# Kernel tuning notes

Hardware: AMD Instinct MI355X
Metric: run time of the kernel (lower is better)

The kernel has to match this reference:

```python
import jax, jax.numpy as jnp
import numpy as np

B, S, D, H, DH, TLEN, TD = 4, 1024, 1024, 16, 64, 256, 256
EPS = 1e-5


def layer_norm(x, g, b):
    m = jnp.mean(x, axis=-1, keepdims=True)
    v = jnp.mean((x - m) ** 2, axis=-1, keepdims=True)
    return (x - m) * jax.lax.rsqrt(v + EPS) * g + b


def rotate_half(x):
    x1, x2 = jnp.split(x, 2, axis=-1)
    return jnp.concatenate((-x2, x1), axis=-1)


def apply_rope(pos, t):
    # pos: [S, DH] -> [1, S, 1, DH]; t: [B, S, H, DH]
    p = pos[None, :, None, :]
    return t * jnp.cos(p) + rotate_half(t) * jnp.sin(p)


def mha(q_in, kv_in, in_w, in_b, out_w, out_b, n_heads):
    # standard nn.MultiheadAttention math (batch-first tensors here)
    d = q_in.shape[-1]
    dh = d // n_heads
    q = q_in @ in_w[:d].T + in_b[:d]
    k = kv_in @ in_w[d:2 * d].T + in_b[d:2 * d]
    v = kv_in @ in_w[2 * d:].T + in_b[2 * d:]
    q = q.reshape(q.shape[0], q.shape[1], n_heads, dh)
    k = k.reshape(k.shape[0], k.shape[1], n_heads, dh)
    v = v.reshape(v.shape[0], v.shape[1], n_heads, dh)
    scores = jnp.einsum('bihd,bjhd->bhij', q, k) / jnp.sqrt(jnp.asarray(dh, q.dtype))
    attn = jax.nn.softmax(scores, axis=-1)
    o = jnp.einsum('bhij,bjhd->bihd', attn, v)
    o = o.reshape(o.shape[0], o.shape[1], d)
    return o @ out_w.T + out_b


def setup_inputs():
    key = jax.random.key(0)
    ks = jax.random.split(key, 20)
    s = 0.02
    inp = {
        'x': jax.random.normal(ks[0], (B, S, D), jnp.float32),
        'text_emb': jax.random.normal(ks[1], (B, TLEN, D), jnp.float32),
        'time_emb': jax.random.normal(ks[2], (B, TD), jnp.float32),
    }
    # true RoPE position encoding, matching RotaryEmbedding.forward
    inv_freq = 1.0 / (10000 ** (jnp.arange(0, DH, 2, dtype=jnp.float32) / DH))
    freqs = jnp.arange(S, dtype=jnp.float32)[:, None] * inv_freq[None, :]
    inp['rotary_pos'] = jnp.concatenate((freqs, freqs), axis=-1)  # [S, DH]
    inp.update(
        ln1_g=jnp.ones((D,), jnp.float32), ln1_b=jnp.zeros((D,), jnp.float32),
        ln2_g=jnp.ones((D,), jnp.float32), ln2_b=jnp.zeros((D,), jnp.float32),
        ln3_g=jnp.ones((D,), jnp.float32), ln3_b=jnp.zeros((D,), jnp.float32),
        attn_in_w=jax.random.normal(ks[3], (3 * D, D), jnp.float32) * s,
        attn_in_b=jnp.zeros((3 * D,), jnp.float32),
        ca_in_w=jax.random.normal(ks[4], (3 * D, D), jnp.float32) * s,
        ca_in_b=jnp.zeros((3 * D,), jnp.float32),
        ca_out_w=jax.random.normal(ks[5], (D, D), jnp.float32) * s,
        ca_out_b=jnp.zeros((D,), jnp.float32),
        fc1_w=jax.random.normal(ks[6], (4 * D, D), jnp.float32) * s,
        fc1_b=jnp.zeros((4 * D,), jnp.float32),
        gate_w=jax.random.normal(ks[7], (4 * D, D), jnp.float32) * s,
        gate_b=jnp.zeros((4 * D,), jnp.float32),
        fc2_w=jax.random.normal(ks[8], (D, 4 * D), jnp.float32) * s,
        fc2_b=jnp.zeros((D,), jnp.float32),
    )
    return inp


def reference(x, text_emb, time_emb, rotary_pos,
              ln1_g, ln1_b, ln2_g, ln2_b, ln3_g, ln3_b,
              attn_in_w, attn_in_b,
              ca_in_w, ca_in_b, ca_out_w, ca_out_b,
              fc1_w, fc1_b, gate_w, gate_b, fc2_w, fc2_b):
    b, n, d = x.shape
    # --- self-attention with manual RoPE (NOTE: original skips out_proj) ---
    residual = x
    xn = layer_norm(x, ln1_g, ln1_b)
    q = xn @ attn_in_w[:d].T + attn_in_b[:d]
    k = xn @ attn_in_w[d:2 * d].T + attn_in_b[d:2 * d]
    v = xn @ attn_in_w[2 * d:].T + attn_in_b[2 * d:]
    q = q.reshape(b, n, H, DH)
    k = k.reshape(b, n, H, DH)
    v = v.reshape(b, n, H, DH)
    q = apply_rope(rotary_pos, q)
    k = apply_rope(rotary_pos, k)
    scores = jnp.einsum('bihd,bjhd->bhij', q, k) / jnp.sqrt(jnp.asarray(DH, x.dtype))
    attn = jax.nn.softmax(scores, axis=-1)
    attn_out = jnp.einsum('bhij,bjhd->bihd', attn, v).reshape(b, n, d)
    x = attn_out + residual
    # --- cross-attention (full MHA, dropout inactive at eval) ---
    residual = x
    xn = layer_norm(x, ln2_g, ln2_b)
    x = mha(xn, text_emb, ca_in_w, ca_in_b, ca_out_w, ca_out_b, H) + residual
    # --- gated MLP ---
    residual = x
    xn = layer_norm(x, ln3_g, ln3_b)
    h = jax.nn.gelu(xn @ fc1_w.T + fc1_b, approximate=False)
    g = jax.nn.sigmoid(xn @ gate_w.T + gate_b)
    return (h * g) @ fc2_w.T + fc2_b + residual
```

## Files before the change

### kernel.cpp

```cpp
#include <hip/hip_runtime.h>
#include <hip/hip_bf16.h>

#define SEQ 1024
#define DIM 1024
#define NH 16

typedef __bf16 bf16_t;
typedef __bf16 bf16x8 __attribute__((ext_vector_type(8)));
typedef __bf16 bf16x4 __attribute__((ext_vector_type(4)));
typedef float f32x4 __attribute__((ext_vector_type(4)));

__device__ __forceinline__ f32x4 mfma16(bf16x8 a, bf16x8 b, f32x4 c) {
    return __builtin_amdgcn_mfma_f32_16x16x32_bf16(a, b, c, 0, 0, 0);
}

__device__ __forceinline__ void gload16(const bf16_t* g, bf16_t* l) {
    __builtin_amdgcn_global_load_lds(
        (const __attribute__((address_space(1))) void*)g,
        (__attribute__((address_space(3))) void*)l, 16, 0, 0);
}

enum { EPI_BF16 = 0, EPI_F32_RESID = 1, EPI_BF16_GELU = 2, EPI_BF16_SIGMUL = 3 };

__global__ __launch_bounds__(256) void cvt_kernel(const float* __restrict__ in,
                                                  bf16_t* __restrict__ out) {
    const int i = blockIdx.x * 256 + threadIdx.x;
    const float4 v = ((const float4*)in)[i];
    bf16x4 o = {(bf16_t)v.x, (bf16_t)v.y, (bf16_t)v.z, (bf16_t)v.w};
    ((bf16x4*)out)[i] = o;
}

__global__ __launch_bounds__(256) void ln_kernel(const float* __restrict__ in,
                                                 const float* __restrict__ g,
                                                 const float* __restrict__ bsh,
                                                 bf16_t* __restrict__ out) {
    __shared__ float red[4], red2[4];
    const int row = blockIdx.x, tid = threadIdx.x;
    const float4 v = ((const float4*)(in + (size_t)row * DIM))[tid];
    float s = v.x + v.y + v.z + v.w;
#pragma unroll
    for (int o = 32; o; o >>= 1) s += __shfl_down(s, o, 64);
    if ((tid & 63) == 0) red[tid >> 6] = s;
    __syncthreads();
    const float mean = (red[0] + red[1] + red[2] + red[3]) * (1.0f / DIM);
    const float dx = v.x - mean, dy = v.y - mean, dz = v.z - mean, dw = v.w - mean;
    float s2 = dx * dx + dy * dy + dz * dz + dw * dw;
#pragma unroll
    for (int o = 32; o; o >>= 1) s2 += __shfl_xor(s2, o, 64);
    if ((tid & 63) == 0) red2[tid >> 6] = s2;
    __syncthreads();
    const float var = (red2[0] + red2[1] + red2[2] + red2[3]) * (1.0f / DIM);
    const float rs = rsqrtf(var + 1e-5f);
    const float4 gv = ((const float4*)g)[tid];
    const float4 bv = ((const float4*)bsh)[tid];
    bf16x4 o4 = {(bf16_t)(dx * rs * gv.x + bv.x), (bf16_t)(dy * rs * gv.y + bv.y),
                 (bf16_t)(dz * rs * gv.z + bv.z), (bf16_t)(dw * rs * gv.w + bv.w)};
    ((bf16x4*)(out + (size_t)row * DIM))[tid] = o4;
}

__global__ __launch_bounds__(256) void rope_kernel(bf16_t* __restrict__ qkv,
                                                   const float* __restrict__ rp) {
    const int t = blockIdx.x * 256 + threadIdx.x;
    const int row = t >> 9;
    const int rem = t & 511;
    const int h = rem >> 5, d = rem & 31;
    const int s = row & (SEQ - 1);
    const float p0 = rp[s * 64 + d];
    const float p1 = rp[s * 64 + d + 32];
    float s0, c0, s1, c1;
    sincosf(p0, &s0, &c0);
    sincosf(p1, &s1, &c1);
    const size_t base = (size_t)row * 3072 + h * 64 + d;
#pragma unroll
    for (int off = 0; off <= 1024; off += 1024) {
        const float a = (float)qkv[base + off];
        const float b = (float)qkv[base + off + 32];
        qkv[base + off] = (bf16_t)(a * c0 - b * s0);
        qkv[base + off + 32] = (bf16_t)(b * c1 + a * s1);
    }
}

__device__ __forceinline__ float epi_apply_gelu(float v) {
    return 0.5f * v * (1.0f + erff(v * 0.70710678118f));
}

template <int EPI>
__global__ __launch_bounds__(512, 4) void gemm8w(
    const bf16_t* __restrict__ A, int lda, const bf16_t* __restrict__ W, int ldw,
    const float* __restrict__ bias, const void* __restrict__ aux,
    void* __restrict__ outv, int ldo, int K, int nM) {
    __shared__ bf16_t As[2][8192];
    __shared__ bf16_t Bs[2][8192];
    const int tid = threadIdx.x;
    const int wave = tid >> 6, lane = tid & 63;
    const int wm = wave >> 2, wn = wave & 3;
    const int lr = lane & 15, hi = lane >> 4;

    const int q = gridDim.x >> 3;
    const int t = (blockIdx.x & 7) * q + (blockIdx.x >> 3);
    const int rowA0 = (t % nM) * 128;
    const int rowB0 = (t / nM) * 128;

    f32x4 acc[4][2];
#pragma unroll
    for (int m = 0; m < 4; ++m)
#pragma unroll
        for (int n = 0; n < 2; ++n) acc[m][n] = (f32x4){0.f, 0.f, 0.f, 0.f};

    const int c0 = wave * 2;
    auto stage = [&](int kt, int b) {
        const int k0 = kt * 64;
#pragma unroll
        for (int u = 0; u < 2; ++u) {
            const int c = c0 + u, s = c >> 1, ks = c & 1;
            const int grow = s * 16 + lr, gcol = k0 + ks * 32 + hi * 8;
            gload16(A + (size_t)(rowA0 + grow) * lda + gcol, &As[b][c * 512]);
            gload16(W + (size_t)(rowB0 + grow) * ldw + gcol, &Bs[b][c * 512]);
        }
    };

    const int NT = K >> 6;
    stage(0, 0);
    __syncthreads();

    for (int kt = 0; kt < NT; ++kt) {
        const int cur = kt & 1;
        if (kt + 1 < NT) stage(kt + 1, cur ^ 1);
#pragma unroll
        for (int ks = 0; ks < 2; ++ks) {
            bf16x8 af[4], bfr[2];
#pragma unroll
            for (int mf = 0; mf < 4; ++mf)
                af[mf] = *(const bf16x8*)&As[cur][((wm * 4 + mf) * 2 + ks) * 512 +
                                                 hi * 128 + lr * 8];
#pragma unroll
            for (int nf = 0; nf < 2; ++nf)
                bfr[nf] = *(const bf16x8*)&Bs[cur][((wn * 2 + nf) * 2 + ks) * 512 +
                                                  hi * 128 + lr * 8];
#pragma unroll
            for (int mf = 0; mf < 4; ++mf)
#pragma unroll
                for (int nf = 0; nf < 2; ++nf)
                    acc[mf][nf] = mfma16(af[mf], bfr[nf], acc[mf][nf]);
        }
        __syncthreads();
    }

    float bn[2];
#pragma unroll
    for (int n = 0; n < 2; ++n) bn[n] = bias[rowB0 + wn * 32 + n * 16 + lr];
#pragma unroll
    for (int m = 0; m < 4; ++m) {
#pragma unroll
        for (int j = 0; j < 4; ++j) {
            const int row = rowA0 + wm * 64 + m * 16 + hi * 4 + j;
#pragma unroll
            for (int n = 0; n < 2; ++n) {
                const int col = rowB0 + wn * 32 + n * 16 + lr;
                float val = acc[m][n][j] + bn[n];
                const size_t oidx = (size_t)row * ldo + col;
                if constexpr (EPI == EPI_BF16) {
                    ((bf16_t*)outv)[oidx] = (bf16_t)val;
                } else if constexpr (EPI == EPI_F32_RESID) {
                    ((float*)outv)[oidx] = val + ((const float*)aux)[oidx];
                } else if constexpr (EPI == EPI_BF16_GELU) {
                    ((bf16_t*)outv)[oidx] = (bf16_t)epi_apply_gelu(val);
                } else {
                    const float sg = 1.0f / (1.0f + expf(-val));
                    ((bf16_t*)outv)[oidx] =
                        (bf16_t)(sg * (float)((const bf16_t*)aux)[oidx]);
                }
            }
        }
    }
}

#define ALD 72
template <bool OUTBF>
__global__ __launch_bounds__(256) void attn_kernel(
    const bf16_t* __restrict__ qp, int ldq, int qoff,
    const bf16_t* __restrict__ kp, int ldk, int koff,
    const bf16_t* __restrict__ vp, int ldv, int voff, int skv,
    const float* __restrict__ resid, void* __restrict__ outp, float scale) {
    __shared__ bf16_t Ks[64 * ALD];
    __shared__ bf16_t Vt[64 * ALD];
    __shared__ bf16_t Ps[4 * 16 * ALD];
    const int b = blockIdx.z, h = blockIdx.y, qt = blockIdx.x;
    const int tid = threadIdx.x;
    const int wave = tid >> 6, lane = tid & 63;
    const int lr = lane & 15, hi = lane >> 4;

    const size_t qrow = (size_t)(b * SEQ + qt * 64 + wave * 16 + lr);
    const bf16_t* qb = qp + qrow * ldq + qoff + h * 64;
    const bf16x8 qf0 = *(const bf16x8*)(qb + hi * 8);
    const bf16x8 qf1 = *(const bf16x8*)(qb + 32 + hi * 8);

    f32x4 oacc[4];
#pragma unroll
    for (int n = 0; n < 4; ++n) oacc[n] = (f32x4){0.f, 0.f, 0.f, 0.f};
    float mrun[4] = {-1e30f, -1e30f, -1e30f, -1e30f};
    float lrun[4] = {0.f, 0.f, 0.f, 0.f};

    bf16_t* pw = &Ps[wave * 16 * ALD];
    const int nkt = skv >> 6;
    for (int kt = 0; kt < nkt; ++kt) {
#pragma unroll
        for (int t = 0; t < 2; ++t) {
            const int idx = t * 256 + tid;
            const int key = idx >> 3, c8 = (idx & 7) * 8;
            const size_t krow = (size_t)(b * skv + kt * 64 + key);
            bf16x8 kv = *(const bf16x8*)(kp + krow * ldk + koff + h * 64 + c8);
            *(bf16x8*)&Ks[key * ALD + c8] = kv;
            bf16x8 vv = *(const bf16x8*)(vp + krow * ldv + voff + h * 64 + c8);
#pragma unroll
            for (int i = 0; i < 8; ++i) Vt[(c8 + i) * ALD + key] = vv[i];
        }
        __syncthreads();

        f32x4 s[4];
#pragma unroll
        for (int n = 0; n < 4; ++n) {
            f32x4 z = (f32x4){0.f, 0.f, 0.f, 0.f};
            z = mfma16(qf0, *(const bf16x8*)&Ks[(n * 16 + lr) * ALD + hi * 8], z);
            z = mfma16(qf1, *(const bf16x8*)&Ks[(n * 16 + lr) * ALD + 32 + hi * 8], z);
            s[n] = z * scale;
        }
        float alpha[4];
#pragma unroll
        for (int j = 0; j < 4; ++j) {
            float mt = fmaxf(fmaxf(s[0][j], s[1][j]), fmaxf(s[2][j], s[3][j]));
#pragma unroll
            for (int o = 8; o >= 1; o >>= 1) mt = fmaxf(mt, __shfl_xor(mt, o, 64));
            const float mnew = fmaxf(mrun[j], mt);
            alpha[j] = expf(mrun[j] - mnew);
            float rsum = 0.f;
#pragma unroll
            for (int n = 0; n < 4; ++n) {
                const float p = expf(s[n][j] - mnew);
                s[n][j] = p;
                rsum += p;
            }
#pragma unroll
            for (int o = 8; o >= 1; o >>= 1) rsum += __shfl_xor(rsum, o, 64);
            lrun[j] = lrun[j] * alpha[j] + rsum;
            mrun[j] = mnew;
        }
#pragma unroll
        for (int j = 0; j < 4; ++j) {
            const int pr = hi * 4 + j;
#pragma unroll
            for (int n = 0; n < 4; ++n) pw[pr * ALD + n * 16 + lr] = (bf16_t)s[n][j];
        }
#pragma unroll
        for (int n = 0; n < 4; ++n)
#pragma unroll
            for (int j = 0; j < 4; ++j) oacc[n][j] *= alpha[j];
#pragma unroll
        for (int ks = 0; ks < 2; ++ks) {
            const bf16x8 pa = *(const bf16x8*)&pw[lr * ALD + ks * 32 + hi * 8];
#pragma unroll
            for (int n = 0; n < 4; ++n) {
                const bf16x8 vf = *(const bf16x8*)&Vt[(n * 16 + lr) * ALD + ks * 32 + hi * 8];
                oacc[n] = mfma16(pa, vf, oacc[n]);
            }
        }
        __syncthreads();
    }

    const size_t orow0 = (size_t)(b * SEQ + qt * 64 + wave * 16);
#pragma unroll
    for (int n = 0; n < 4; ++n) {
#pragma unroll
        for (int j = 0; j < 4; ++j) {
            const int r = hi * 4 + j;
            const size_t idx = (orow0 + r) * DIM + h * 64 + n * 16 + lr;
            float val = oacc[n][j] / lrun[j];
            if constexpr (OUTBF) {
                ((bf16_t*)outp)[idx] = (bf16_t)val;
            } else {
                ((float*)outp)[idx] = val + resid[idx];
            }
        }
    }
}

extern "C" void kernel_launch(void* const* d_in, const int* in_sizes, int n_in,
                              void* d_out, int out_size, void* d_ws, size_t ws_size,
                              hipStream_t stream) {
    const float* x = (const float*)d_in[0];
    const float* text_emb = (const float*)d_in[1];
    const float* rotary = (const float*)d_in[3];
    const float* ln1_g = (const float*)d_in[4];
    const float* ln1_b = (const float*)d_in[5];
    const float* ln2_g = (const float*)d_in[6];
    const float* ln2_b = (const float*)d_in[7];
    const float* ln3_g = (const float*)d_in[8];
    const float* ln3_b = (const float*)d_in[9];
    const float* attn_in_w = (const float*)d_in[10];
    const float* attn_in_b = (const float*)d_in[11];
    const float* ca_in_w = (const float*)d_in[12];
    const float* ca_in_b = (const float*)d_in[13];
    const float* ca_out_w = (const float*)d_in[14];
    const float* ca_out_b = (const float*)d_in[15];
    const float* fc1_w = (const float*)d_in[16];
    const float* fc1_b = (const float*)d_in[17];
    const float* gate_w = (const float*)d_in[18];
    const float* gate_b = (const float*)d_in[19];
    const float* fc2_w = (const float*)d_in[20];
    const float* fc2_b = (const float*)d_in[21];

    char* ws = (char*)d_ws;
    bf16_t* attn_w_bf = (bf16_t*)(ws);
    bf16_t* ca_in_bf = (bf16_t*)(ws + 6291456);
    bf16_t* ca_out_bf = (bf16_t*)(ws + 12582912);
    bf16_t* fc1_bf = (bf16_t*)(ws + 14680064);
    bf16_t* gate_bf = (bf16_t*)(ws + 23068672);
    bf16_t* fc2_bf = (bf16_t*)(ws + 31457280);
    bf16_t* text_bf = (bf16_t*)(ws + 39845888);
    bf16_t* xn = (bf16_t*)(ws + 41943040);
    float* xA = (float*)(ws + 50331648);
    char* S = ws + 67108864;
    bf16_t* qkv = (bf16_t*)S;
    bf16_t* cq = (bf16_t*)S;
    bf16_t* ckv = (bf16_t*)(S + 8388608);
    bf16_t* ca_attn = (bf16_t*)(S + 12582912);
    bf16_t* hbuf = (bf16_t*)S;
    float* out = (float*)d_out;

    cvt_kernel<<<3072, 256, 0, stream>>>(attn_in_w, attn_w_bf);
    cvt_kernel<<<3072, 256, 0, stream>>>(ca_in_w, ca_in_bf);
    cvt_kernel<<<1024, 256, 0, stream>>>(ca_out_w, ca_out_bf);
    cvt_kernel<<<4096, 256, 0, stream>>>(fc1_w, fc1_bf);
    cvt_kernel<<<4096, 256, 0, stream>>>(gate_w, gate_bf);
    cvt_kernel<<<4096, 256, 0, stream>>>(fc2_w, fc2_bf);
    cvt_kernel<<<1024, 256, 0, stream>>>(text_emb, text_bf);

    ln_kernel<<<4096, 256, 0, stream>>>(x, ln1_g, ln1_b, xn);
    gemm8w<EPI_BF16><<<768, 512, 0, stream>>>(
        xn, 1024, attn_w_bf, 1024, attn_in_b, nullptr, qkv, 3072, 1024, 32);
    rope_kernel<<<8192, 256, 0, stream>>>(qkv, rotary);
    attn_kernel<false><<<dim3(16, 16, 4), 256, 0, stream>>>(
        qkv, 3072, 0, qkv, 3072, 1024, qkv, 3072, 2048, 1024, x, xA, 0.125f);

    ln_kernel<<<4096, 256, 0, stream>>>(xA, ln2_g, ln2_b, xn);
    gemm8w<EPI_BF16><<<256, 512, 0, stream>>>(
        xn, 1024, ca_in_bf, 1024, ca_in_b, nullptr, cq, 1024, 1024, 32);
    gemm8w<EPI_BF16><<<128, 512, 0, stream>>>(
        text_bf, 1024, ca_in_bf + (size_t)1024 * 1024, 1024, ca_in_b + 1024, nullptr,
        ckv, 2048, 1024, 8);
    attn_kernel<true><<<dim3(16, 16, 4), 256, 0, stream>>>(
        cq, 1024, 0, ckv, 2048, 0, ckv, 2048, 1024, 256, nullptr, ca_attn, 0.125f);
    gemm8w<EPI_F32_RESID><<<256, 512, 0, stream>>>(
        ca_attn, 1024, ca_out_bf, 1024, ca_out_b, xA, xA, 1024, 1024, 32);

    ln_kernel<<<4096, 256, 0, stream>>>(xA, ln3_g, ln3_b, xn);
    gemm8w<EPI_BF16_GELU><<<1024, 512, 0, stream>>>(
        xn, 1024, fc1_bf, 1024, fc1_b, nullptr, hbuf, 4096, 1024, 32);
    gemm8w<EPI_BF16_SIGMUL><<<1024, 512, 0, stream>>>(
        xn, 1024, gate_bf, 1024, gate_b, hbuf, hbuf, 4096, 1024, 32);
    gemm8w<EPI_F32_RESID><<<256, 512, 0, stream>>>(
        hbuf, 4096, fc2_bf, 4096, fc2_b, xA, out, 1024, 4096, 32);
}
```

Measured before the change: 569.8 us.

## Pre-transpose V and stream K/V tiles into LDS via direct global loads

Adds a separate kernel that transposes V per head into a [b,h,d,s] buffer, so the attention kernel no longer performs scalar transposed LDS stores per tile. The new attention kernel loads K and V tiles with global_load_lds in an MFMA-friendly swizzled layout, remaps block indices for better L2 locality across heads, and switches to fast __expf. This adds an extra kernel launch and a round trip through global memory for V, and the direct LDS loads are not double-buffered.

```diff
diff --git a/kernel.cpp b/kernel.cpp
--- a/kernel.cpp
+++ b/kernel.cpp
@@ -82,6 +82,148 @@
 
 __device__ __forceinline__ float epi_apply_gelu(float v) {
     return 0.5f * v * (1.0f + erff(v * 0.70710678118f));
+}
+
+__global__ __launch_bounds__(256) void vtrans_kernel(
+    const bf16_t* __restrict__ src, int ld, int voff, int skv,
+    bf16_t* __restrict__ vt) {
+    __shared__ bf16_t T[64 * 72];
+    const int qt = blockIdx.x, h = blockIdx.y, b = blockIdx.z;
+    const int tid = threadIdx.x;
+    const int s0 = qt * 64;
+#pragma unroll
+    for (int t = 0; t < 2; ++t) {
+        const int idx = t * 256 + tid;
+        const int r = idx >> 3, c8 = (idx & 7) * 8;
+        bf16x8 v = *(const bf16x8*)(src + (size_t)(b * skv + s0 + r) * ld +
+                                    voff + h * 64 + c8);
+        *(bf16x8*)&T[r * 72 + c8] = v;
+    }
+    __syncthreads();
+    const size_t base = ((size_t)(b * NH + h) * 64) * skv;
+#pragma unroll
+    for (int t = 0; t < 2; ++t) {
+        const int idx = t * 256 + tid;
+        const int d = idx >> 3, s8 = (idx & 7) * 8;
+        bf16x8 w;
+#pragma unroll
+        for (int i = 0; i < 8; ++i) w[i] = T[(s8 + i) * 72 + d];
+        *(bf16x8*)(vt + base + (size_t)d * skv + s0 + s8) = w;
+    }
+}
+
+#define ALD 72
+template <bool OUTBF>
+__global__ __launch_bounds__(256) void attn2_kernel(
+    const bf16_t* __restrict__ qp, int ldq, int qoff,
+    const bf16_t* __restrict__ kp, int ldk, int koff,
+    const bf16_t* __restrict__ vtp, int skv,
+    const float* __restrict__ resid, void* __restrict__ outp, float scale) {
+    __shared__ bf16_t Ks[4096];
+    __shared__ bf16_t Vs[4096];
+    __shared__ bf16_t Ps[4 * 16 * ALD];
+    const int nwg = gridDim.x;
+    const int t = (blockIdx.x & 7) * (nwg >> 3) + (blockIdx.x >> 3);
+    const int qt = t & 15;
+    const int bh = t >> 4;
+    const int b = bh >> 4, h = bh & 15;
+    const int tid = threadIdx.x;
+    const int wave = tid >> 6, lane = tid & 63;
+    const int lr = lane & 15, hi = lane >> 4;
+
+    const size_t qrow = (size_t)(b * SEQ + qt * 64 + wave * 16 + lr);
+    const bf16_t* qb = qp + qrow * ldq + qoff + h * 64;
+    const bf16x8 qf0 = *(const bf16x8*)(qb + hi * 8);
+    const bf16x8 qf1 = *(const bf16x8*)(qb + 32 + hi * 8);
+
+    const bf16_t* vbase = vtp + ((size_t)bh * 64) * skv;
+
+    f32x4 oacc[4];
+#pragma unroll
+    for (int n = 0; n < 4; ++n) oacc[n] = (f32x4){0.f, 0.f, 0.f, 0.f};
+    float mrun[4] = {-1e30f, -1e30f, -1e30f, -1e30f};
+    float lrun[4] = {0.f, 0.f, 0.f, 0.f};
+
+    bf16_t* pw = &Ps[wave * 16 * ALD];
+    const int nkt = skv >> 6;
+    for (int kt = 0; kt < nkt; ++kt) {
+#pragma unroll
+        for (int u = 0; u < 2; ++u) {
+            const int c = wave * 2 + u;
+            const int grow = wave * 16 + lr, gcol = u * 32 + hi * 8;
+            gload16(kp + (size_t)(b * skv + kt * 64 + grow) * ldk + koff +
+                        h * 64 + gcol,
+                    &Ks[c * 512]);
+            gload16(vbase + (size_t)grow * skv + kt * 64 + gcol, &Vs[c * 512]);
+        }
+        __syncthreads();
+
+        f32x4 s[4];
+#pragma unroll
+        for (int n = 0; n < 4; ++n) {
+            f32x4 z = (f32x4){0.f, 0.f, 0.f, 0.f};
+            z = mfma16(qf0, *(const bf16x8*)&Ks[(n * 2 + 0) * 512 + hi * 128 + lr * 8], z);
+            z = mfma16(qf1, *(const bf16x8*)&Ks[(n * 2 + 1) * 512 + hi * 128 + lr * 8], z);
+            s[n] = z * scale;
+        }
+        float alpha[4];
+#pragma unroll
+        for (int j = 0; j < 4; ++j) {
+            float mt = fmaxf(fmaxf(s[0][j], s[1][j]), fmaxf(s[2][j], s[3][j]));
+#pragma unroll
+            for (int o = 8; o >= 1; o >>= 1) mt = fmaxf(mt, __shfl_xor(mt, o, 64));
+            const float mnew = fmaxf(mrun[j], mt);
+            alpha[j] = __expf(mrun[j] - mnew);
+            float rsum = 0.f;
+#pragma unroll
+            for (int n = 0; n < 4; ++n) {
+                const float p = __expf(s[n][j] - mnew);
+                s[n][j] = p;
+                rsum += p;
+            }
+#pragma unroll
+            for (int o = 8; o >= 1; o >>= 1) rsum += __shfl_xor(rsum, o, 64);
+            lrun[j] = lrun[j] * alpha[j] + rsum;
+            mrun[j] = mnew;
+        }
+#pragma unroll
+        for (int j = 0; j < 4; ++j) {
+            const int pr = hi * 4 + j;
+#pragma unroll
+            for (int n = 0; n < 4; ++n) pw[pr * ALD + n * 16 + lr] = (bf16_t)s[n][j];
+        }
+#pragma unroll
+        for (int n = 0; n < 4; ++n)
+#pragma unroll
+            for (int j = 0; j < 4; ++j) oacc[n][j] *= alpha[j];
+#pragma unroll
+        for (int ks = 0; ks < 2; ++ks) {
+            const bf16x8 pa = *(const bf16x8*)&pw[lr * ALD + ks * 32 + hi * 8];
+#pragma unroll
+            for (int n = 0; n < 4; ++n) {
+                const bf16x8 vf =
+                    *(const bf16x8*)&Vs[(n * 2 + ks) * 512 + hi * 128 + lr * 8];
+                oacc[n] = mfma16(pa, vf, oacc[n]);
+            }
+        }
+        __syncthreads();
+    }
+
+    const size_t orow0 = (size_t)(b * SEQ + qt * 64 + wave * 16);
+#pragma unroll
+    for (int n = 0; n < 4; ++n) {
+#pragma unroll
+        for (int j = 0; j < 4; ++j) {
+            const int r = hi * 4 + j;
+            const size_t idx = (orow0 + r) * DIM + h * 64 + n * 16 + lr;
+            float val = oacc[n][j] / lrun[j];
+            if constexpr (OUTBF) {
+                ((bf16_t*)outp)[idx] = (bf16_t)val;
+            } else {
+                ((float*)outp)[idx] = val + resid[idx];
+            }
+        }
+    }
 }
 
 template <int EPI>
@@ -170,115 +312,6 @@
                     ((bf16_t*)outv)[oidx] =
                         (bf16_t)(sg * (float)((const bf16_t*)aux)[oidx]);
                 }
-            }
-        }
-    }
-}
-
-#define ALD 72
-template <bool OUTBF>
-__global__ __launch_bounds__(256) void attn_kernel(
-    const bf16_t* __restrict__ qp, int ldq, int qoff,
-    const bf16_t* __restrict__ kp, int ldk, int koff,
-    const bf16_t* __restrict__ vp, int ldv, int voff, int skv,
-    const float* __restrict__ resid, void* __restrict__ outp, float scale) {
-    __shared__ bf16_t Ks[64 * ALD];
-    __shared__ bf16_t Vt[64 * ALD];
-    __shared__ bf16_t Ps[4 * 16 * ALD];
-    const int b = blockIdx.z, h = blockIdx.y, qt = blockIdx.x;
-    const int tid = threadIdx.x;
-    const int wave = tid >> 6, lane = tid & 63;
-    const int lr = lane & 15, hi = lane >> 4;
-
-    const size_t qrow = (size_t)(b * SEQ + qt * 64 + wave * 16 + lr);
-    const bf16_t* qb = qp + qrow * ldq + qoff + h * 64;
-    const bf16x8 qf0 = *(const bf16x8*)(qb + hi * 8);
-    const bf16x8 qf1 = *(const bf16x8*)(qb + 32 + hi * 8);
-
-    f32x4 oacc[4];
-#pragma unroll
-    for (int n = 0; n < 4; ++n) oacc[n] = (f32x4){0.f, 0.f, 0.f, 0.f};
-    float mrun[4] = {-1e30f, -1e30f, -1e30f, -1e30f};
-    float lrun[4] = {0.f, 0.f, 0.f, 0.f};
-
-    bf16_t* pw = &Ps[wave * 16 * ALD];
-    const int nkt = skv >> 6;
-    for (int kt = 0; kt < nkt; ++kt) {
-#pragma unroll
-        for (int t = 0; t < 2; ++t) {
-            const int idx = t * 256 + tid;
-            const int key = idx >> 3, c8 = (idx & 7) * 8;
-            const size_t krow = (size_t)(b * skv + kt * 64 + key);
-            bf16x8 kv = *(const bf16x8*)(kp + krow * ldk + koff + h * 64 + c8);
-            *(bf16x8*)&Ks[key * ALD + c8] = kv;
-            bf16x8 vv = *(const bf16x8*)(vp + krow * ldv + voff + h * 64 + c8);
-#pragma unroll
-            for (int i = 0; i < 8; ++i) Vt[(c8 + i) * ALD + key] = vv[i];
-        }
-        __syncthreads();
-
-        f32x4 s[4];
-#pragma unroll
-        for (int n = 0; n < 4; ++n) {
-            f32x4 z = (f32x4){0.f, 0.f, 0.f, 0.f};
-            z = mfma16(qf0, *(const bf16x8*)&Ks[(n * 16 + lr) * ALD + hi * 8], z);
-            z = mfma16(qf1, *(const bf16x8*)&Ks[(n * 16 + lr) * ALD + 32 + hi * 8], z);
-            s[n] = z * scale;
-        }
-        float alpha[4];
-#pragma unroll
-        for (int j = 0; j < 4; ++j) {
-            float mt = fmaxf(fmaxf(s[0][j], s[1][j]), fmaxf(s[2][j], s[3][j]));
-#pragma unroll
-            for (int o = 8; o >= 1; o >>= 1) mt = fmaxf(mt, __shfl_xor(mt, o, 64));
-            const float mnew = fmaxf(mrun[j], mt);
-            alpha[j] = expf(mrun[j] - mnew);
-            float rsum = 0.f;
-#pragma unroll
-            for (int n = 0; n < 4; ++n) {
-                const float p = expf(s[n][j] - mnew);
-                s[n][j] = p;
-                rsum += p;
-            }
-#pragma unroll
-            for (int o = 8; o >= 1; o >>= 1) rsum += __shfl_xor(rsum, o, 64);
-            lrun[j] = lrun[j] * alpha[j] + rsum;
-            mrun[j] = mnew;
-        }
-#pragma unroll
-        for (int j = 0; j < 4; ++j) {
-            const int pr = hi * 4 + j;
-#pragma unroll
-            for (int n = 0; n < 4; ++n) pw[pr * ALD + n * 16 + lr] = (bf16_t)s[n][j];
-        }
-#pragma unroll
-        for (int n = 0; n < 4; ++n)
-#pragma unroll
-            for (int j = 0; j < 4; ++j) oacc[n][j] *= alpha[j];
-#pragma unroll
-        for (int ks = 0; ks < 2; ++ks) {
-            const bf16x8 pa = *(const bf16x8*)&pw[lr * ALD + ks * 32 + hi * 8];
-#pragma unroll
-            for (int n = 0; n < 4; ++n) {
-                const bf16x8 vf = *(const bf16x8*)&Vt[(n * 16 + lr) * ALD + ks * 32 + hi * 8];
-                oacc[n] = mfma16(pa, vf, oacc[n]);
-            }
-        }
-        __syncthreads();
-    }
-
-    const size_t orow0 = (size_t)(b * SEQ + qt * 64 + wave * 16);
-#pragma unroll
-    for (int n = 0; n < 4; ++n) {
-#pragma unroll
-        for (int j = 0; j < 4; ++j) {
-            const int r = hi * 4 + j;
-            const size_t idx = (orow0 + r) * DIM + h * 64 + n * 16 + lr;
-            float val = oacc[n][j] / lrun[j];
-            if constexpr (OUTBF) {
-                ((bf16_t*)outp)[idx] = (bf16_t)val;
-            } else {
-                ((float*)outp)[idx] = val + resid[idx];
             }
         }
     }
@@ -321,9 +354,11 @@
     float* xA = (float*)(ws + 50331648);
     char* S = ws + 67108864;
     bf16_t* qkv = (bf16_t*)S;
+    bf16_t* vtSelf = (bf16_t*)(S + 25165824);
     bf16_t* cq = (bf16_t*)S;
     bf16_t* ckv = (bf16_t*)(S + 8388608);
     bf16_t* ca_attn = (bf16_t*)(S + 12582912);
+    bf16_t* vtCross = (bf16_t*)(S + 20971520);
     bf16_t* hbuf = (bf16_t*)S;
     float* out = (float*)d_out;
 
@@ -339,8 +374,9 @@
     gemm8w<EPI_BF16><<<768, 512, 0, stream>>>(
         xn, 1024, attn_w_bf, 1024, attn_in_b, nullptr, qkv, 3072, 1024, 32);
     rope_kernel<<<8192, 256, 0, stream>>>(qkv, rotary);
-    attn_kernel<false><<<dim3(16, 16, 4), 256, 0, stream>>>(
-        qkv, 3072, 0, qkv, 3072, 1024, qkv, 3072, 2048, 1024, x, xA, 0.125f);
+    vtrans_kernel<<<dim3(16, 16, 4), 256, 0, stream>>>(qkv, 3072, 2048, 1024, vtSelf);
+    attn2_kernel<false><<<1024, 256, 0, stream>>>(
+        qkv, 3072, 0, qkv, 3072, 1024, vtSelf, 1024, x, xA, 0.125f);
 
     ln_kernel<<<4096, 256, 0, stream>>>(xA, ln2_g, ln2_b, xn);
     gemm8w<EPI_BF16><<<256, 512, 0, stream>>>(
@@ -348,8 +384,9 @@
     gemm8w<EPI_BF16><<<128, 512, 0, stream>>>(
         text_bf, 1024, ca_in_bf + (size_t)1024 * 1024, 1024, ca_in_b + 1024, nullptr,
         ckv, 2048, 1024, 8);
-    attn_kernel<true><<<dim3(16, 16, 4), 256, 0, stream>>>(
-        cq, 1024, 0, ckv, 2048, 0, ckv, 2048, 1024, 256, nullptr, ca_attn, 0.125f);
+    vtrans_kernel<<<dim3(4, 16, 4), 256, 0, stream>>>(ckv, 2048, 1024, 256, vtCross);
+    attn2_kernel<true><<<1024, 256, 0, stream>>>(
+        cq, 1024, 0, ckv, 2048, 0, vtCross, 256, nullptr, ca_attn, 0.125f);
     gemm8w<EPI_F32_RESID><<<256, 512, 0, stream>>>(
         ca_attn, 1024, ca_out_bf, 1024, ca_out_b, xA, xA, 1024, 1024, 32);
 
```

Result: faster. 534.4 us (-6.2%).
